# Optimization experiments

Hardware: AMD Instinct MI355X
Metric: run time of the kernel (lower is better)

Reference implementation:

```python
import jax, jax.numpy as jnp
import numpy as np
from jax.scipy.special import logsumexp

B, T, H, L = 64, 512, 768, 9


def setup_inputs() -> dict:
    key = jax.random.key(0)
    ks = jax.random.split(key, 8)
    length = jax.random.randint(ks[0], (B,), 0, T, dtype=jnp.int32)
    word2vec = jax.random.normal(ks[1], (B, T, H), dtype=jnp.float32)
    mask = jnp.ones((B, T), dtype=jnp.int32)
    label = jax.random.randint(ks[2], (B, T), 0, L, dtype=jnp.int32)
    # Linear(768 -> num_labels) params (PyTorch default init scale)
    bound = 1.0 / np.sqrt(H)
    W = jax.random.uniform(ks[3], (L, H), jnp.float32, -bound, bound)
    b = jax.random.uniform(ks[4], (L,), jnp.float32, -bound, bound)
    # CRF params (torchcrf init: uniform(-0.1, 0.1))
    start_transitions = jax.random.uniform(ks[5], (L,), jnp.float32, -0.1, 0.1)
    end_transitions = jax.random.uniform(ks[6], (L,), jnp.float32, -0.1, 0.1)
    transitions = jax.random.uniform(ks[7], (L, L), jnp.float32, -0.1, 0.1)
    return {"length": length, "word2vec": word2vec, "mask": mask, "label": label,
            "W": W, "b": b, "start_transitions": start_transitions,
            "end_transitions": end_transitions, "transitions": transitions}


def _crf_nll(emissions, tags, mask, start_transitions, end_transitions, transitions):
    # emissions [B,T,L], tags [B,T] int, mask [B,T] {0,1}
    Bn, Tn, Ln = emissions.shape
    maskf = mask.astype(emissions.dtype)
    # ---- numerator: score of the given tag sequence ----
    batch = jnp.arange(Bn)
    score = start_transitions[tags[:, 0]] + emissions[batch, 0, tags[:, 0]]
    # transition scores for steps 1..T-1, vectorized over time
    trans_sc = transitions[tags[:, :-1], tags[:, 1:]]                    # [B,T-1]
    emit_sc = jnp.take_along_axis(emissions, tags[..., None], axis=2)[..., 0]  # [B,T]
    score = score + jnp.sum((trans_sc + emit_sc[:, 1:]) * maskf[:, 1:], axis=1)
    seq_ends = jnp.sum(mask, axis=1).astype(jnp.int32) - 1
    last_tags = tags[batch, seq_ends]
    numerator = score + end_transitions[last_tags]
    # ---- denominator: log partition via forward algorithm (scan over time) ----
    em_t = jnp.transpose(emissions, (1, 0, 2))   # [T,B,L]
    mk_t = jnp.transpose(mask, (1, 0)) != 0      # [T,B]
    alpha0 = start_transitions[None, :] + em_t[0]  # [B,L]

    def step(alpha, inp):
        em_i, m_i = inp
        # alpha[b, i] + transitions[i, j] + emissions[b, j]
        nxt = logsumexp(alpha[:, :, None] + transitions[None, :, :] + em_i[:, None, :], axis=1)
        alpha = jnp.where(m_i[:, None], nxt, alpha)
        return alpha, None

    alpha, _ = jax.lax.scan(step, alpha0, (em_t[1:], mk_t[1:]))
    denominator = logsumexp(alpha + end_transitions[None, :], axis=1)
    llh = numerator - denominator
    return -jnp.mean(llh)


def reference(length, word2vec, mask, label, W, b, start_transitions, end_transitions, transitions):
    # dropout p=0.0 -> identity; Linear projection to emissions
    emissions = jnp.einsum('bth,lh->btl', word2vec, W) + b  # [B,T,L]
    return _crf_nll(emissions, label, mask, start_transitions, end_transitions, transitions)
```

## Files before the change

kernel.cpp:

```cpp
#include <hip/hip_runtime.h>
#include <hip/hip_bf16.h>


#define Bn 64
#define Tn 512
#define Hn 768
#define Ln 9
#define EMS 12
#define CS 16
#define NCHQ 8
#define QT 128
#define KSTEPS 24

typedef short bf16x8 __attribute__((ext_vector_type(8)));
typedef float f32x4  __attribute__((ext_vector_type(4)));

__device__ __forceinline__ short f2bf(float f) {
    return (short)__builtin_bit_cast(unsigned short, __float2bfloat16(f));
}

__global__ __launch_bounds__(512) void emis_q_kernel(
    const float* __restrict__ wv, const float* __restrict__ Wm,
    const float* __restrict__ bias, const int* __restrict__ mask,
    const int* __restrict__ label, const float* __restrict__ trans,
    const float* __restrict__ startT,
    float* __restrict__ Mq, float* __restrict__ lgq,
    float* __restrict__ numq, int* __restrict__ msq,
    float* __restrict__ em0, int* __restrict__ cnt)
{
    __shared__ bf16x8 wlds[KSTEPS * 64];
    __shared__ float  ldsE[QT][EMS];
    __shared__ int    ldsM[QT];
    __shared__ float  eTs[81];
    __shared__ float  sM[NCHQ][Ln][Ln];
    __shared__ float  sLg[NCHQ][Ln];
    __shared__ float  sp[8];
    __shared__ int    si[8];

    const int tid   = threadIdx.x;
    const int lane  = tid & 63;
    const int wid   = tid >> 6;
    const int bid   = blockIdx.x;
    const int b     = bid >> 2;
    const int q     = bid & 3;
    const int tbase = q * QT;

    if (bid == 0 && tid == 0) cnt[0] = 0;
    if (tid < 81) eTs[tid] = __expf(trans[tid]);

    for (int idx = tid; idx < KSTEPS * 64; idx += 512) {
        const int kk = idx >> 6, ln = idx & 63;
        const int n = ln & 15, kb2 = ln >> 4;
        bf16x8 v;
        if (n < Ln) {
            const float* src = Wm + n * Hn + kk * 32 + kb2 * 8;
#pragma unroll
            for (int j = 0; j < 8; ++j) v[j] = f2bf(src[j]);
        } else {
#pragma unroll
            for (int j = 0; j < 8; ++j) v[j] = 0;
        }
        wlds[idx] = v;
    }
    __syncthreads();

    {
        const int m  = lane & 15;
        const int kb = lane >> 4;
        const float* abase = wv + (size_t)(bid * QT + wid * 16 + m) * Hn + kb * 8;

        f32x4 acc = {0.f, 0.f, 0.f, 0.f};
#pragma unroll 4
        for (int kk = 0; kk < KSTEPS; ++kk) {
            float4 x0 = *reinterpret_cast<const float4*>(abase + kk * 32);
            float4 x1 = *reinterpret_cast<const float4*>(abase + kk * 32 + 4);
            bf16x8 a;
            a[0] = f2bf(x0.x); a[1] = f2bf(x0.y); a[2] = f2bf(x0.z); a[3] = f2bf(x0.w);
            a[4] = f2bf(x1.x); a[5] = f2bf(x1.y); a[6] = f2bf(x1.z); a[7] = f2bf(x1.w);
            bf16x8 bfr = wlds[kk * 64 + lane];
            acc = __builtin_amdgcn_mfma_f32_16x16x32_bf16(a, bfr, acc, 0, 0, 0);
        }
        const int l = lane & 15;
        if (l < Ln) {
            const float bl = bias[l];
#pragma unroll
            for (int r = 0; r < 4; ++r) {
                const int lrow = wid * 16 + (lane >> 4) * 4 + r;
                ldsE[lrow][l] = __expf(acc[r] + bl);
            }
        }
    }
    __syncthreads();

    float part = 0.f; int ms = 0;
    if (tid < QT) {
        const int gt  = tbase + tid;
        const int tag = label[b * Tn + gt];
        const int mk  = mask[b * Tn + gt];
        ldsM[tid] = mk; ms = mk;
        if (gt == 0) {
            part = startT[tag] + __logf(ldsE[0][tag]);
        } else if (mk) {
            const int prev = label[b * Tn + gt - 1];
            part = trans[prev * Ln + tag] + __logf(ldsE[tid][tag]);
        }
    }
#pragma unroll
    for (int off = 32; off > 0; off >>= 1) {
        part += __shfl_xor(part, off);
        ms   += __shfl_xor(ms, off);
    }
    if (lane == 0) { sp[wid] = part; si[wid] = ms; }
    __syncthreads();

    if (tid < NCHQ * Ln) {
        float Tr[81];
#pragma unroll
        for (int i = 0; i < 81; ++i) Tr[i] = eTs[i];
        const int r = tid % Ln;
        const int c = tid / Ln;

        float v[9];
#pragma unroll
        for (int k = 0; k < 9; ++k) v[k] = (k == r) ? 1.f : 0.f;
        float lg = 0.f;

        int t0 = tbase + c * CS; if (t0 == 0) t0 = 1;
        const int t1 = tbase + (c + 1) * CS;

        int lt = t0 - tbase;
        float4 e0v = *reinterpret_cast<const float4*>(&ldsE[lt][0]);
        float4 e1v = *reinterpret_cast<const float4*>(&ldsE[lt][4]);
        float  e8  = ldsE[lt][8];
        int    mk  = ldsM[lt];

        for (int t = t0; t < t1; ++t) {
            float4 p0 = make_float4(0.f, 0.f, 0.f, 0.f), p1 = p0;
            float  p8 = 0.f; int pm = 0;
            if (t + 1 < t1) {
                const int nlt = t + 1 - tbase;
                p0 = *reinterpret_cast<const float4*>(&ldsE[nlt][0]);
                p1 = *reinterpret_cast<const float4*>(&ldsE[nlt][4]);
                p8 = ldsE[nlt][8];
                pm = ldsM[nlt];
            }
            if (mk) {
                float e[9] = {e0v.x, e0v.y, e0v.z, e0v.w, e1v.x, e1v.y, e1v.z, e1v.w, e8};
                float nv[9];
#pragma unroll
                for (int jj = 0; jj < 9; ++jj) {
                    float acc = v[0] * Tr[jj];
#pragma unroll
                    for (int k = 1; k < 9; ++k) acc += v[k] * Tr[k * 9 + jj];
                    nv[jj] = acc * e[jj];
                }
                float mx = nv[0];
#pragma unroll
                for (int jj = 1; jj < 9; ++jj) mx = fmaxf(mx, nv[jj]);
                float inv = 1.f / mx;
#pragma unroll
                for (int jj = 0; jj < 9; ++jj) v[jj] = nv[jj] * inv;
                lg += __logf(mx);
            }
            e0v = p0; e1v = p1; e8 = p8; mk = pm;
        }
#pragma unroll
        for (int jj = 0; jj < 9; ++jj) sM[c][r][jj] = v[jj];
        sLg[c][r] = lg;
    }
    if (q == 0 && tid >= 72 && tid < 81) em0[b * Ln + (tid - 72)] = ldsE[0][tid - 72];
    if (tid == 100) {
        float s = 0.f; int m2 = 0;
#pragma unroll
        for (int i = 0; i < 8; ++i) { s += sp[i]; m2 += si[i]; }
        numq[bid] = s; msq[bid] = m2;
    }
    __syncthreads();

    for (int n = 4; n >= 2; n >>= 1) {
        float vout[9]; float lgout = 0.f;
        const bool act = tid < n * Ln;
        int p = 0, r = 0;
        if (act) {
            p = tid / Ln; r = tid % Ln;
            float mB = sLg[2 * p + 1][0];
#pragma unroll
            for (int k = 1; k < 9; ++k) mB = fmaxf(mB, sLg[2 * p + 1][k]);
            float tA[9];
#pragma unroll
            for (int k = 0; k < 9; ++k) tA[k] = sM[2 * p][r][k] * __expf(sLg[2 * p + 1][k] - mB);
#pragma unroll
            for (int jj = 0; jj < 9; ++jj) {
                float acc = tA[0] * sM[2 * p + 1][0][jj];
#pragma unroll
                for (int k = 1; k < 9; ++k) acc += tA[k] * sM[2 * p + 1][k][jj];
                vout[jj] = acc;
            }
            float mx = vout[0];
#pragma unroll
            for (int jj = 1; jj < 9; ++jj) mx = fmaxf(mx, vout[jj]);
            float inv = 1.f / mx;
#pragma unroll
            for (int jj = 0; jj < 9; ++jj) vout[jj] *= inv;
            lgout = sLg[2 * p][r] + mB + __logf(mx);
        }
        __syncthreads();
        if (act) {
#pragma unroll
            for (int jj = 0; jj < 9; ++jj) sM[p][r][jj] = vout[jj];
            sLg[p][r] = lgout;
        }
        __syncthreads();
    }

    if (tid < Ln) {
        const int r = tid;
        float mB = sLg[1][0];
#pragma unroll
        for (int k = 1; k < 9; ++k) mB = fmaxf(mB, sLg[1][k]);
        float tA[9];
#pragma unroll
        for (int k = 0; k < 9; ++k) tA[k] = sM[0][r][k] * __expf(sLg[1][k] - mB);
        float v[9];
#pragma unroll
        for (int jj = 0; jj < 9; ++jj) {
            float acc = tA[0] * sM[1][0][jj];
#pragma unroll
            for (int k = 1; k < 9; ++k) acc += tA[k] * sM[1][k][jj];
            v[jj] = acc;
        }
        float mx = v[0];
#pragma unroll
        for (int jj = 1; jj < 9; ++jj) mx = fmaxf(mx, v[jj]);
        float inv = 1.f / mx;
#pragma unroll
        for (int jj = 0; jj < 9; ++jj) Mq[bid * 81 + r * 9 + jj] = v[jj] * inv;
        lgq[bid * Ln + r] = sLg[0][r] + mB + __logf(mx);
    }
}

__global__ __launch_bounds__(64) void comb_kernel(
    const float* __restrict__ Mq, const float* __restrict__ lgq,
    const float* __restrict__ numq, const int* __restrict__ msq,
    const float* __restrict__ em0, const int* __restrict__ label,
    const float* __restrict__ startT, const float* __restrict__ endT,
    float* __restrict__ partial, int* __restrict__ cnt, float* __restrict__ out)
{
    __shared__ float cM[4][Ln][Ln];
    __shared__ float cLg[4][Ln];
    __shared__ float cem[Ln];
    __shared__ float cnum[4];
    __shared__ int   cms[4];

    const int b = blockIdx.x, tid = threadIdx.x;

    for (int i = tid; i < 4 * 81; i += 64) cM[i / 81][(i % 81) / 9][i % 9] = Mq[b * 324 + i];
    for (int i = tid; i < 4 * 9; i += 64)  cLg[i / 9][i % 9] = lgq[b * 36 + i];
    if (tid < Ln) cem[tid] = em0[b * Ln + tid];
    if (tid < 4) { cnum[tid] = numq[b * 4 + tid]; cms[tid] = msq[b * 4 + tid]; }
    __syncthreads();

    if (tid < 16) {
        const int lj = tid;
        const float NEG = -1e30f;
        float la = (lj < Ln) ? (startT[lj] + __logf(cem[lj])) : NEG;
        for (int c = 0; c < 4; ++c) {
            float mc[9];
#pragma unroll
            for (int rr = 0; rr < 9; ++rr) mc[rr] = (lj < Ln) ? cM[c][rr][lj] : 0.f;
            float x = (lj < Ln) ? (la + cLg[c][lj]) : NEG;
            float mm = x;
#pragma unroll
            for (int off = 1; off < 16; off <<= 1) mm = fmaxf(mm, __shfl_xor(mm, off, 16));
            float w = __expf(x - mm);
            float sacc = 0.f;
#pragma unroll
            for (int rr = 0; rr < 9; ++rr) sacc += __shfl(w, rr, 16) * mc[rr];
            la = (lj < Ln) ? (mm + __logf(sacc)) : NEG;
        }
        float x = (lj < Ln) ? (la + endT[lj]) : NEG;
        float mm = x;
#pragma unroll
        for (int off = 1; off < 16; off <<= 1) mm = fmaxf(mm, __shfl_xor(mm, off, 16));
        float se = __expf(x - mm);
#pragma unroll
        for (int off = 1; off < 16; off <<= 1) se += __shfl_xor(se, off, 16);
        if (lj == 0) {
            float denom = mm + __logf(se);
            float numer = cnum[0] + cnum[1] + cnum[2] + cnum[3];
            int   sm    = cms[0] + cms[1] + cms[2] + cms[3];
            int   last  = label[b * Tn + sm - 1];
            partial[b]  = denom - (numer + endT[last]);
        }
    }

    int old = 0;
    if (tid == 0) {
        __threadfence();
        old = atomicAdd(cnt, 1);
    }
    old = __shfl(old, 0);
    if (old == Bn - 1) {
        __threadfence();
        float pv = partial[tid];
#pragma unroll
        for (int off = 32; off > 0; off >>= 1) pv += __shfl_xor(pv, off);
        if (tid == 0) out[0] = pv * (1.0f / Bn);
    }
}

extern "C" void kernel_launch(void* const* d_in, const int* in_sizes, int n_in,
                              void* d_out, int out_size, void* d_ws, size_t ws_size,
                              hipStream_t stream)
{
    const float* wv    = (const float*)d_in[1];
    const int*   mask  = (const int*)d_in[2];
    const int*   label = (const int*)d_in[3];
    const float* Wm    = (const float*)d_in[4];
    const float* bias  = (const float*)d_in[5];
    const float* st    = (const float*)d_in[6];
    const float* en    = (const float*)d_in[7];
    const float* tr    = (const float*)d_in[8];

    float* ws      = (float*)d_ws;
    float* Mq      = ws;
    float* lgq     = ws + 20736;
    float* numq    = ws + 23040;
    int*   msq     = (int*)(ws + 23296);
    float* em0     = ws + 23552;
    float* partial = ws + 24128;
    int*   cnt     = (int*)(ws + 24192);
    float* out     = (float*)d_out;

    hipLaunchKernelGGL(emis_q_kernel, dim3(256), dim3(512), 0, stream,
                       wv, Wm, bias, mask, label, tr, st,
                       Mq, lgq, numq, msq, em0, cnt);
    hipLaunchKernelGGL(comb_kernel, dim3(Bn), dim3(64), 0, stream,
                       Mq, lgq, numq, msq, em0, label, st, en,
                       partial, cnt, out);
}
```

Before: 40.07 us.

## Split work into eighths and stream activations via async global-to-LDS triple buffer

Each batch row is now split into 8 blocks of 64 timesteps with 256 threads, doubling the block count so all CUs are covered. The activation loads now use global_load_lds into a swizzled, triple-buffered LDS ring with explicit waitcnt, which overlaps memory fetch with the MFMA projection. The chunk scan and tree combine are confined to wave 0 without block barriers, and the combine kernel gains one extra pairwise level. The cost is more LDS per block, more intermediate data in the workspace, and hand-written waitcnt counts that must match the issued loads exactly.

```diff
diff --git a/kernel.cpp b/kernel.cpp
--- a/kernel.cpp
+++ b/kernel.cpp
@@ -8,8 +8,8 @@
 #define Ln 9
 #define EMS 12
 #define CS 16
-#define NCHQ 8
-#define QT 128
+#define NCHO 4
+#define OT 64
 #define KSTEPS 24
 
 typedef short bf16x8 __attribute__((ext_vector_type(8)));
@@ -19,7 +19,40 @@
     return (short)__builtin_bit_cast(unsigned short, __float2bfloat16(f));
 }
 
-__global__ __launch_bounds__(512) void emis_q_kernel(
+#define GLOAD16(gp, lp)                                                        \
+    __builtin_amdgcn_global_load_lds(                                          \
+        (const __attribute__((address_space(1))) void*)(gp),                   \
+        (__attribute__((address_space(3))) void*)(lp), 16, 0, 0)
+
+__device__ __forceinline__ void pair_combine(
+    const float (*MA)[Ln], const float* lgA,
+    const float (*MB)[Ln], const float* lgB,
+    int r, float* outM, float* outLg)
+{
+    float mB = lgB[0];
+#pragma unroll
+    for (int k = 1; k < 9; ++k) mB = fmaxf(mB, lgB[k]);
+    float tA[9];
+#pragma unroll
+    for (int k = 0; k < 9; ++k) tA[k] = MA[r][k] * __expf(lgB[k] - mB);
+    float v[9];
+#pragma unroll
+    for (int jj = 0; jj < 9; ++jj) {
+        float acc = tA[0] * MB[0][jj];
+#pragma unroll
+        for (int k = 1; k < 9; ++k) acc += tA[k] * MB[k][jj];
+        v[jj] = acc;
+    }
+    float mx = v[0];
+#pragma unroll
+    for (int jj = 1; jj < 9; ++jj) mx = fmaxf(mx, v[jj]);
+    float inv = 1.f / mx;
+#pragma unroll
+    for (int jj = 0; jj < 9; ++jj) outM[jj] = v[jj] * inv;
+    *outLg = lgA[r] + mB + __logf(mx);
+}
+
+__global__ __launch_bounds__(256) void emis_o_kernel(
     const float* __restrict__ wv, const float* __restrict__ Wm,
     const float* __restrict__ bias, const int* __restrict__ mask,
     const int* __restrict__ label, const float* __restrict__ trans,
@@ -29,26 +62,27 @@
     float* __restrict__ em0, int* __restrict__ cnt)
 {
     __shared__ bf16x8 wlds[KSTEPS * 64];
-    __shared__ float  ldsE[QT][EMS];
-    __shared__ int    ldsM[QT];
-    __shared__ float  eTs[81];
-    __shared__ float  sM[NCHQ][Ln][Ln];
-    __shared__ float  sLg[NCHQ][Ln];
-    __shared__ float  sp[8];
-    __shared__ int    si[8];
+    __shared__ __align__(16) float bufA[4][3][512];
+    __shared__ float ldsE[OT][EMS];
+    __shared__ int   ldsM[OT];
+    __shared__ float eTs[81];
+    __shared__ float sM[NCHO][Ln][Ln];
+    __shared__ float sLg[NCHO][Ln];
+    __shared__ float s2M[2][Ln][Ln];
+    __shared__ float s2Lg[2][Ln];
 
     const int tid   = threadIdx.x;
     const int lane  = tid & 63;
     const int wid   = tid >> 6;
     const int bid   = blockIdx.x;
-    const int b     = bid >> 2;
-    const int q     = bid & 3;
-    const int tbase = q * QT;
+    const int b     = bid >> 3;
+    const int o     = bid & 7;
+    const int tbase = o * OT;
 
     if (bid == 0 && tid == 0) cnt[0] = 0;
     if (tid < 81) eTs[tid] = __expf(trans[tid]);
 
-    for (int idx = tid; idx < KSTEPS * 64; idx += 512) {
+    for (int idx = tid; idx < KSTEPS * 64; idx += 256) {
         const int kk = idx >> 6, ln = idx & 63;
         const int n = ln & 15, kb2 = ln >> 4;
         bf16x8 v;
@@ -65,21 +99,50 @@
     __syncthreads();
 
     {
+        const int rowbase = bid * OT + wid * 16;
+        const int rr   = lane >> 3;
+        const int colf = (((lane & 7) * 16) ^ (rr << 4)) >> 2;
+        const float* g0 = wv + (size_t)(rowbase + rr) * Hn + colf;
+        const float* g1 = g0 + 8 * Hn;
+        float* lb = &bufA[wid][0][0];
+
         const int m  = lane & 15;
         const int kb = lane >> 4;
-        const float* abase = wv + (size_t)(bid * QT + wid * 16 + m) * Hn + kb * 8;
+        const int ph0 = m * 32 + (((kb * 32)      ^ ((m & 7) << 4)) >> 2);
+        const int ph1 = m * 32 + (((kb * 32 + 16) ^ ((m & 7) << 4)) >> 2);
 
         f32x4 acc = {0.f, 0.f, 0.f, 0.f};
-#pragma unroll 4
-        for (int kk = 0; kk < KSTEPS; ++kk) {
-            float4 x0 = *reinterpret_cast<const float4*>(abase + kk * 32);
-            float4 x1 = *reinterpret_cast<const float4*>(abase + kk * 32 + 4);
-            bf16x8 a;
-            a[0] = f2bf(x0.x); a[1] = f2bf(x0.y); a[2] = f2bf(x0.z); a[3] = f2bf(x0.w);
-            a[4] = f2bf(x1.x); a[5] = f2bf(x1.y); a[6] = f2bf(x1.z); a[7] = f2bf(x1.w);
-            bf16x8 bfr = wlds[kk * 64 + lane];
-            acc = __builtin_amdgcn_mfma_f32_16x16x32_bf16(a, bfr, acc, 0, 0, 0);
-        }
+
+        GLOAD16(g0,      lb);        GLOAD16(g1,      lb + 256);
+        GLOAD16(g0 + 32, lb + 512);  GLOAD16(g1 + 32, lb + 768);
+
+#define EMIS_STEP(KK, SLOT)                                                    \
+        {                                                                      \
+            const float* s_ = lb + (SLOT) * 512;                               \
+            float4 x0 = *reinterpret_cast<const float4*>(s_ + ph0);            \
+            float4 x1 = *reinterpret_cast<const float4*>(s_ + ph1);            \
+            bf16x8 a;                                                          \
+            a[0] = f2bf(x0.x); a[1] = f2bf(x0.y);                              \
+            a[2] = f2bf(x0.z); a[3] = f2bf(x0.w);                              \
+            a[4] = f2bf(x1.x); a[5] = f2bf(x1.y);                              \
+            a[6] = f2bf(x1.z); a[7] = f2bf(x1.w);                              \
+            bf16x8 bfr = wlds[(KK) * 64 + lane];                               \
+            acc = __builtin_amdgcn_mfma_f32_16x16x32_bf16(a, bfr, acc, 0, 0, 0); \
+        }
+
+        for (int kk = 0; kk < KSTEPS - 2; ++kk) {
+            const int sl2 = (kk + 2) % 3;
+            GLOAD16(g0 + (kk + 2) * 32, lb + sl2 * 512);
+            GLOAD16(g1 + (kk + 2) * 32, lb + sl2 * 512 + 256);
+            asm volatile("s_waitcnt vmcnt(4)" ::: "memory");
+            EMIS_STEP(kk, kk % 3);
+        }
+        asm volatile("s_waitcnt vmcnt(2)" ::: "memory");
+        EMIS_STEP(KSTEPS - 2, (KSTEPS - 2) % 3);
+        asm volatile("s_waitcnt vmcnt(0)" ::: "memory");
+        EMIS_STEP(KSTEPS - 1, (KSTEPS - 1) % 3);
+#undef EMIS_STEP
+
         const int l = lane & 15;
         if (l < Ln) {
             const float bl = bias[l];
@@ -92,150 +155,101 @@
     }
     __syncthreads();
 
-    float part = 0.f; int ms = 0;
-    if (tid < QT) {
-        const int gt  = tbase + tid;
+    if (wid == 0) {
+        const int gt  = tbase + lane;
         const int tag = label[b * Tn + gt];
         const int mk  = mask[b * Tn + gt];
-        ldsM[tid] = mk; ms = mk;
+        ldsM[lane] = mk;
+        float part = 0.f; int ms = mk;
         if (gt == 0) {
             part = startT[tag] + __logf(ldsE[0][tag]);
         } else if (mk) {
             const int prev = label[b * Tn + gt - 1];
-            part = trans[prev * Ln + tag] + __logf(ldsE[tid][tag]);
-        }
-    }
-#pragma unroll
-    for (int off = 32; off > 0; off >>= 1) {
-        part += __shfl_xor(part, off);
-        ms   += __shfl_xor(ms, off);
-    }
-    if (lane == 0) { sp[wid] = part; si[wid] = ms; }
-    __syncthreads();
-
-    if (tid < NCHQ * Ln) {
-        float Tr[81];
-#pragma unroll
-        for (int i = 0; i < 81; ++i) Tr[i] = eTs[i];
-        const int r = tid % Ln;
-        const int c = tid / Ln;
-
-        float v[9];
-#pragma unroll
-        for (int k = 0; k < 9; ++k) v[k] = (k == r) ? 1.f : 0.f;
-        float lg = 0.f;
-
-        int t0 = tbase + c * CS; if (t0 == 0) t0 = 1;
-        const int t1 = tbase + (c + 1) * CS;
-
-        int lt = t0 - tbase;
-        float4 e0v = *reinterpret_cast<const float4*>(&ldsE[lt][0]);
-        float4 e1v = *reinterpret_cast<const float4*>(&ldsE[lt][4]);
-        float  e8  = ldsE[lt][8];
-        int    mk  = ldsM[lt];
-
-        for (int t = t0; t < t1; ++t) {
-            float4 p0 = make_float4(0.f, 0.f, 0.f, 0.f), p1 = p0;
-            float  p8 = 0.f; int pm = 0;
-            if (t + 1 < t1) {
-                const int nlt = t + 1 - tbase;
-                p0 = *reinterpret_cast<const float4*>(&ldsE[nlt][0]);
-                p1 = *reinterpret_cast<const float4*>(&ldsE[nlt][4]);
-                p8 = ldsE[nlt][8];
-                pm = ldsM[nlt];
+            part = trans[prev * Ln + tag] + __logf(ldsE[lane][tag]);
+        }
+#pragma unroll
+        for (int off = 32; off > 0; off >>= 1) {
+            part += __shfl_xor(part, off);
+            ms   += __shfl_xor(ms, off);
+        }
+        if (lane == 0) { numq[bid] = part; msq[bid] = ms; }
+        if (o == 0 && lane < Ln) em0[b * Ln + lane] = ldsE[0][lane];
+
+        if (tid < NCHO * Ln) {
+            float Tr[81];
+#pragma unroll
+            for (int i = 0; i < 81; ++i) Tr[i] = eTs[i];
+            const int r = tid % Ln;
+            const int c = tid / Ln;
+
+            float v[9];
+#pragma unroll
+            for (int k = 0; k < 9; ++k) v[k] = (k == r) ? 1.f : 0.f;
+            float lg = 0.f;
+
+            int t0 = tbase + c * CS; if (t0 == 0) t0 = 1;
+            const int t1 = tbase + (c + 1) * CS;
+
+            int lt = t0 - tbase;
+            float4 e0v = *reinterpret_cast<const float4*>(&ldsE[lt][0]);
+            float4 e1v = *reinterpret_cast<const float4*>(&ldsE[lt][4]);
+            float  e8  = ldsE[lt][8];
+            int    mk2 = ldsM[lt];
+
+            for (int t = t0; t < t1; ++t) {
+                float4 p0 = make_float4(0.f, 0.f, 0.f, 0.f), p1 = p0;
+                float  p8 = 0.f; int pm = 0;
+                if (t + 1 < t1) {
+                    const int nlt = t + 1 - tbase;
+                    p0 = *reinterpret_cast<const float4*>(&ldsE[nlt][0]);
+                    p1 = *reinterpret_cast<const float4*>(&ldsE[nlt][4]);
+                    p8 = ldsE[nlt][8];
+                    pm = ldsM[nlt];
+                }
+                if (mk2) {
+                    float e[9] = {e0v.x, e0v.y, e0v.z, e0v.w,
+                                  e1v.x, e1v.y, e1v.z, e1v.w, e8};
+                    float nv[9];
+#pragma unroll
+                    for (int jj = 0; jj < 9; ++jj) {
+                        float acc = v[0] * Tr[jj];
+#pragma unroll
+                        for (int k = 1; k < 9; ++k) acc += v[k] * Tr[k * 9 + jj];
+                        nv[jj] = acc * e[jj];
+                    }
+                    float mx = nv[0];
+#pragma unroll
+                    for (int jj = 1; jj < 9; ++jj) mx = fmaxf(mx, nv[jj]);
+                    float inv = 1.f / mx;
+#pragma unroll
+                    for (int jj = 0; jj < 9; ++jj) v[jj] = nv[jj] * inv;
+                    lg += __logf(mx);
+                }
+                e0v = p0; e1v = p1; e8 = p8; mk2 = pm;
             }
-            if (mk) {
-                float e[9] = {e0v.x, e0v.y, e0v.z, e0v.w, e1v.x, e1v.y, e1v.z, e1v.w, e8};
-                float nv[9];
-#pragma unroll
-                for (int jj = 0; jj < 9; ++jj) {
-                    float acc = v[0] * Tr[jj];
-#pragma unroll
-                    for (int k = 1; k < 9; ++k) acc += v[k] * Tr[k * 9 + jj];
-                    nv[jj] = acc * e[jj];
-                }
-                float mx = nv[0];
-#pragma unroll
-                for (int jj = 1; jj < 9; ++jj) mx = fmaxf(mx, nv[jj]);
-                float inv = 1.f / mx;
-#pragma unroll
-                for (int jj = 0; jj < 9; ++jj) v[jj] = nv[jj] * inv;
-                lg += __logf(mx);
-            }
-            e0v = p0; e1v = p1; e8 = p8; mk = pm;
-        }
-#pragma unroll
-        for (int jj = 0; jj < 9; ++jj) sM[c][r][jj] = v[jj];
-        sLg[c][r] = lg;
-    }
-    if (q == 0 && tid >= 72 && tid < 81) em0[b * Ln + (tid - 72)] = ldsE[0][tid - 72];
-    if (tid == 100) {
-        float s = 0.f; int m2 = 0;
-#pragma unroll
-        for (int i = 0; i < 8; ++i) { s += sp[i]; m2 += si[i]; }
-        numq[bid] = s; msq[bid] = m2;
-    }
-    __syncthreads();
-
-    for (int n = 4; n >= 2; n >>= 1) {
-        float vout[9]; float lgout = 0.f;
-        const bool act = tid < n * Ln;
-        int p = 0, r = 0;
-        if (act) {
-            p = tid / Ln; r = tid % Ln;
-            float mB = sLg[2 * p + 1][0];
-#pragma unroll
-            for (int k = 1; k < 9; ++k) mB = fmaxf(mB, sLg[2 * p + 1][k]);
-            float tA[9];
-#pragma unroll
-            for (int k = 0; k < 9; ++k) tA[k] = sM[2 * p][r][k] * __expf(sLg[2 * p + 1][k] - mB);
-#pragma unroll
-            for (int jj = 0; jj < 9; ++jj) {
-                float acc = tA[0] * sM[2 * p + 1][0][jj];
-#pragma unroll
-                for (int k = 1; k < 9; ++k) acc += tA[k] * sM[2 * p + 1][k][jj];
-                vout[jj] = acc;
-            }
-            float mx = vout[0];
-#pragma unroll
-            for (int jj = 1; jj < 9; ++jj) mx = fmaxf(mx, vout[jj]);
-            float inv = 1.f / mx;
-#pragma unroll
-            for (int jj = 0; jj < 9; ++jj) vout[jj] *= inv;
-            lgout = sLg[2 * p][r] + mB + __logf(mx);
-        }
-        __syncthreads();
-        if (act) {
-#pragma unroll
-            for (int jj = 0; jj < 9; ++jj) sM[p][r][jj] = vout[jj];
-            sLg[p][r] = lgout;
-        }
-        __syncthreads();
-    }
-
-    if (tid < Ln) {
-        const int r = tid;
-        float mB = sLg[1][0];
-#pragma unroll
-        for (int k = 1; k < 9; ++k) mB = fmaxf(mB, sLg[1][k]);
-        float tA[9];
-#pragma unroll
-        for (int k = 0; k < 9; ++k) tA[k] = sM[0][r][k] * __expf(sLg[1][k] - mB);
-        float v[9];
-#pragma unroll
-        for (int jj = 0; jj < 9; ++jj) {
-            float acc = tA[0] * sM[1][0][jj];
-#pragma unroll
-            for (int k = 1; k < 9; ++k) acc += tA[k] * sM[1][k][jj];
-            v[jj] = acc;
-        }
-        float mx = v[0];
-#pragma unroll
-        for (int jj = 1; jj < 9; ++jj) mx = fmaxf(mx, v[jj]);
-        float inv = 1.f / mx;
-#pragma unroll
-        for (int jj = 0; jj < 9; ++jj) Mq[bid * 81 + r * 9 + jj] = v[jj] * inv;
-        lgq[bid * Ln + r] = sLg[0][r] + mB + __logf(mx);
+#pragma unroll
+            for (int jj = 0; jj < 9; ++jj) sM[c][r][jj] = v[jj];
+            sLg[c][r] = lg;
+        }
+
+        if (tid < 2 * Ln) {
+            const int p = tid / Ln, r = tid % Ln;
+            float om[9], ol;
+            pair_combine(sM[2 * p], sLg[2 * p], sM[2 * p + 1], sLg[2 * p + 1],
+                         r, om, &ol);
+#pragma unroll
+            for (int jj = 0; jj < 9; ++jj) s2M[p][r][jj] = om[jj];
+            s2Lg[p][r] = ol;
+        }
+
+        if (tid < Ln) {
+            const int r = tid;
+            float om[9], ol;
+            pair_combine(s2M[0], s2Lg[0], s2M[1], s2Lg[1], r, om, &ol);
+#pragma unroll
+            for (int jj = 0; jj < 9; ++jj) Mq[bid * 81 + r * 9 + jj] = om[jj];
+            lgq[bid * Ln + r] = ol;
+        }
     }
 }
 
@@ -246,18 +260,31 @@
     const float* __restrict__ startT, const float* __restrict__ endT,
     float* __restrict__ partial, int* __restrict__ cnt, float* __restrict__ out)
 {
-    __shared__ float cM[4][Ln][Ln];
-    __shared__ float cLg[4][Ln];
+    __shared__ float cO[8][Ln][Ln];
+    __shared__ float cOl[8][Ln];
+    __shared__ float cQ[4][Ln][Ln];
+    __shared__ float cQl[4][Ln];
     __shared__ float cem[Ln];
-    __shared__ float cnum[4];
-    __shared__ int   cms[4];
+    __shared__ float cnum[8];
+    __shared__ int   cms[8];
 
     const int b = blockIdx.x, tid = threadIdx.x;
 
-    for (int i = tid; i < 4 * 81; i += 64) cM[i / 81][(i % 81) / 9][i % 9] = Mq[b * 324 + i];
-    for (int i = tid; i < 4 * 9; i += 64)  cLg[i / 9][i % 9] = lgq[b * 36 + i];
+    for (int i = tid; i < 8 * 81; i += 64) ((float*)cO)[i]  = Mq[b * 648 + i];
+    for (int i = tid; i < 8 * 9;  i += 64) ((float*)cOl)[i] = lgq[b * 72 + i];
     if (tid < Ln) cem[tid] = em0[b * Ln + tid];
-    if (tid < 4) { cnum[tid] = numq[b * 4 + tid]; cms[tid] = msq[b * 4 + tid]; }
+    if (tid < 8) { cnum[tid] = numq[b * 8 + tid]; cms[tid] = msq[b * 8 + tid]; }
+    __syncthreads();
+
+    if (tid < 4 * Ln) {
+        const int p = tid / Ln, r = tid % Ln;
+        float om[9], ol;
+        pair_combine(cO[2 * p], cOl[2 * p], cO[2 * p + 1], cOl[2 * p + 1],
+                     r, om, &ol);
+#pragma unroll
+        for (int jj = 0; jj < 9; ++jj) cQ[p][r][jj] = om[jj];
+        cQl[p][r] = ol;
+    }
     __syncthreads();
 
     if (tid < 16) {
@@ -267,8 +294,8 @@
         for (int c = 0; c < 4; ++c) {
             float mc[9];
 #pragma unroll
-            for (int rr = 0; rr < 9; ++rr) mc[rr] = (lj < Ln) ? cM[c][rr][lj] : 0.f;
-            float x = (lj < Ln) ? (la + cLg[c][lj]) : NEG;
+            for (int rr = 0; rr < 9; ++rr) mc[rr] = (lj < Ln) ? cQ[c][rr][lj] : 0.f;
+            float x = (lj < Ln) ? (la + cQl[c][lj]) : NEG;
             float mm = x;
 #pragma unroll
             for (int off = 1; off < 16; off <<= 1) mm = fmaxf(mm, __shfl_xor(mm, off, 16));
@@ -287,8 +314,10 @@
         for (int off = 1; off < 16; off <<= 1) se += __shfl_xor(se, off, 16);
         if (lj == 0) {
             float denom = mm + __logf(se);
-            float numer = cnum[0] + cnum[1] + cnum[2] + cnum[3];
-            int   sm    = cms[0] + cms[1] + cms[2] + cms[3];
+            float numer = cnum[0] + cnum[1] + cnum[2] + cnum[3]
+                        + cnum[4] + cnum[5] + cnum[6] + cnum[7];
+            int   sm    = cms[0] + cms[1] + cms[2] + cms[3]
+                        + cms[4] + cms[5] + cms[6] + cms[7];
             int   last  = label[b * Tn + sm - 1];
             partial[b]  = denom - (numer + endT[last]);
         }
@@ -324,15 +353,15 @@
 
     float* ws      = (float*)d_ws;
     float* Mq      = ws;
-    float* lgq     = ws + 20736;
-    float* numq    = ws + 23040;
-    int*   msq     = (int*)(ws + 23296);
-    float* em0     = ws + 23552;
-    float* partial = ws + 24128;
-    int*   cnt     = (int*)(ws + 24192);
+    float* lgq     = ws + 41472;
+    float* numq    = ws + 46080;
+    int*   msq     = (int*)(ws + 46592);
+    float* em0     = ws + 47104;
+    float* partial = ws + 47680;
+    int*   cnt     = (int*)(ws + 47744);
     float* out     = (float*)d_out;
 
-    hipLaunchKernelGGL(emis_q_kernel, dim3(256), dim3(512), 0, stream,
+    hipLaunchKernelGGL(emis_o_kernel, dim3(512), dim3(256), 0, stream,
                        wv, Wm, bias, mask, label, tr, st,
                        Mq, lgq, numq, msq, em0, cnt);
     hipLaunchKernelGGL(comb_kernel, dim3(Bn), dim3(64), 0, stream,
```

Result: slower. 42.21 us (+5.3%).

## Fuse combine kernel into main kernel via last-block atomic counter

Applied to the files above, without the earlier changes.

Removes the separate combine kernel launch. Each block increments a global counter with release semantics, and the last block to arrive does the per-sequence chunk combination for all 64 batches and the final mean reduction. A hipMemsetAsync resets the counter before launch. The intent is to drop a kernel launch and the gap between kernels. The cost is that a single block serializes the combine work, and the memset adds its own operation to the stream.

```diff
diff --git a/kernel.cpp b/kernel.cpp
--- a/kernel.cpp
+++ b/kernel.cpp
@@ -11,6 +11,7 @@
 #define NCHQ 8
 #define QT 128
 #define KSTEPS 24
+#define NBLKS 256
 
 typedef short bf16x8 __attribute__((ext_vector_type(8)));
 typedef float f32x4  __attribute__((ext_vector_type(4)));
@@ -23,10 +24,11 @@
     const float* __restrict__ wv, const float* __restrict__ Wm,
     const float* __restrict__ bias, const int* __restrict__ mask,
     const int* __restrict__ label, const float* __restrict__ trans,
-    const float* __restrict__ startT,
+    const float* __restrict__ startT, const float* __restrict__ endT,
     float* __restrict__ Mq, float* __restrict__ lgq,
     float* __restrict__ numq, int* __restrict__ msq,
-    float* __restrict__ em0, int* __restrict__ cnt)
+    float* __restrict__ em0, int* __restrict__ cnt,
+    float* __restrict__ out)
 {
     __shared__ bf16x8 wlds[KSTEPS * 64];
     __shared__ float  ldsE[QT][EMS];
@@ -36,6 +38,8 @@
     __shared__ float  sLg[NCHQ][Ln];
     __shared__ float  sp[8];
     __shared__ int    si[8];
+    __shared__ float  nllArr[Bn];
+    __shared__ int    sOld;
 
     const int tid   = threadIdx.x;
     const int lane  = tid & 63;
@@ -45,7 +49,6 @@
     const int q     = bid & 3;
     const int tbase = q * QT;
 
-    if (bid == 0 && tid == 0) cnt[0] = 0;
     if (tid < 81) eTs[tid] = __expf(trans[tid]);
 
     for (int idx = tid; idx < KSTEPS * 64; idx += 512) {
@@ -237,72 +240,65 @@
         for (int jj = 0; jj < 9; ++jj) Mq[bid * 81 + r * 9 + jj] = v[jj] * inv;
         lgq[bid * Ln + r] = sLg[0][r] + mB + __logf(mx);
     }
-}
-
-__global__ __launch_bounds__(64) void comb_kernel(
-    const float* __restrict__ Mq, const float* __restrict__ lgq,
-    const float* __restrict__ numq, const int* __restrict__ msq,
-    const float* __restrict__ em0, const int* __restrict__ label,
-    const float* __restrict__ startT, const float* __restrict__ endT,
-    float* __restrict__ partial, int* __restrict__ cnt, float* __restrict__ out)
-{
-    __shared__ float cM[4][Ln][Ln];
-    __shared__ float cLg[4][Ln];
-    __shared__ float cem[Ln];
-    __shared__ float cnum[4];
-    __shared__ int   cms[4];
-
-    const int b = blockIdx.x, tid = threadIdx.x;
-
-    for (int i = tid; i < 4 * 81; i += 64) cM[i / 81][(i % 81) / 9][i % 9] = Mq[b * 324 + i];
-    for (int i = tid; i < 4 * 9; i += 64)  cLg[i / 9][i % 9] = lgq[b * 36 + i];
-    if (tid < Ln) cem[tid] = em0[b * Ln + tid];
-    if (tid < 4) { cnum[tid] = numq[b * 4 + tid]; cms[tid] = msq[b * 4 + tid]; }
-    __syncthreads();
-
-    if (tid < 16) {
-        const int lj = tid;
+
+    __syncthreads();
+    if (tid == 0) {
+        sOld = __hip_atomic_fetch_add(cnt, 1, __ATOMIC_RELEASE,
+                                      __HIP_MEMORY_SCOPE_AGENT);
+    }
+    __syncthreads();
+    if (sOld != NBLKS - 1) return;
+
+    if (tid == 0) {
+        (void)__hip_atomic_load(cnt, __ATOMIC_ACQUIRE, __HIP_MEMORY_SCOPE_AGENT);
+    }
+    __syncthreads();
+
+    {
+        const int lj = tid & 15;
+        const int g  = tid >> 4;
         const float NEG = -1e30f;
-        float la = (lj < Ln) ? (startT[lj] + __logf(cem[lj])) : NEG;
-        for (int c = 0; c < 4; ++c) {
-            float mc[9];
-#pragma unroll
-            for (int rr = 0; rr < 9; ++rr) mc[rr] = (lj < Ln) ? cM[c][rr][lj] : 0.f;
-            float x = (lj < Ln) ? (la + cLg[c][lj]) : NEG;
+#pragma unroll
+        for (int pass = 0; pass < 2; ++pass) {
+            const int bb = g + pass * 32;
+            float la = (lj < Ln) ? (startT[lj] + __logf(em0[bb * Ln + lj])) : NEG;
+            for (int c = 0; c < 4; ++c) {
+                const float* Mc = Mq + (bb * 4 + c) * 81;
+                float mc[9];
+#pragma unroll
+                for (int rr = 0; rr < 9; ++rr) mc[rr] = (lj < Ln) ? Mc[rr * 9 + lj] : 0.f;
+                float x = (lj < Ln) ? (la + lgq[(bb * 4 + c) * Ln + lj]) : NEG;
+                float mm = x;
+#pragma unroll
+                for (int off = 1; off < 16; off <<= 1) mm = fmaxf(mm, __shfl_xor(mm, off, 16));
+                float w = __expf(x - mm);
+                float sacc = 0.f;
+#pragma unroll
+                for (int rr = 0; rr < 9; ++rr) sacc += __shfl(w, rr, 16) * mc[rr];
+                la = (lj < Ln) ? (mm + __logf(sacc)) : NEG;
+            }
+            float x = (lj < Ln) ? (la + endT[lj]) : NEG;
             float mm = x;
 #pragma unroll
             for (int off = 1; off < 16; off <<= 1) mm = fmaxf(mm, __shfl_xor(mm, off, 16));
-            float w = __expf(x - mm);
-            float sacc = 0.f;
-#pragma unroll
-            for (int rr = 0; rr < 9; ++rr) sacc += __shfl(w, rr, 16) * mc[rr];
-            la = (lj < Ln) ? (mm + __logf(sacc)) : NEG;
-        }
-        float x = (lj < Ln) ? (la + endT[lj]) : NEG;
-        float mm = x;
-#pragma unroll
-        for (int off = 1; off < 16; off <<= 1) mm = fmaxf(mm, __shfl_xor(mm, off, 16));
-        float se = __expf(x - mm);
-#pragma unroll
-        for (int off = 1; off < 16; off <<= 1) se += __shfl_xor(se, off, 16);
-        if (lj == 0) {
-            float denom = mm + __logf(se);
-            float numer = cnum[0] + cnum[1] + cnum[2] + cnum[3];
-            int   sm    = cms[0] + cms[1] + cms[2] + cms[3];
-            int   last  = label[b * Tn + sm - 1];
-            partial[b]  = denom - (numer + endT[last]);
-        }
-    }
-
-    int old = 0;
-    if (tid == 0) {
-        __threadfence();
-        old = atomicAdd(cnt, 1);
-    }
-    old = __shfl(old, 0);
-    if (old == Bn - 1) {
-        __threadfence();
-        float pv = partial[tid];
+            float se = __expf(x - mm);
+#pragma unroll
+            for (int off = 1; off < 16; off <<= 1) se += __shfl_xor(se, off, 16);
+            if (lj == 0) {
+                float denom = mm + __logf(se);
+                float numer = numq[bb * 4 + 0] + numq[bb * 4 + 1]
+                            + numq[bb * 4 + 2] + numq[bb * 4 + 3];
+                int   sm    = msq[bb * 4 + 0] + msq[bb * 4 + 1]
+                            + msq[bb * 4 + 2] + msq[bb * 4 + 3];
+                int   last  = label[bb * Tn + sm - 1];
+                nllArr[bb]  = denom - (numer + endT[last]);
+            }
+        }
+    }
+    __syncthreads();
+
+    if (tid < 64) {
+        float pv = nllArr[tid];
 #pragma unroll
         for (int off = 32; off > 0; off >>= 1) pv += __shfl_xor(pv, off);
         if (tid == 0) out[0] = pv * (1.0f / Bn);
@@ -328,14 +324,12 @@
     float* numq    = ws + 23040;
     int*   msq     = (int*)(ws + 23296);
     float* em0     = ws + 23552;
-    float* partial = ws + 24128;
-    int*   cnt     = (int*)(ws + 24192);
+    int*   cnt     = (int*)(ws + 24128);
     float* out     = (float*)d_out;
 
-    hipLaunchKernelGGL(emis_q_kernel, dim3(256), dim3(512), 0, stream,
-                       wv, Wm, bias, mask, label, tr, st,
-                       Mq, lgq, numq, msq, em0, cnt);
-    hipLaunchKernelGGL(comb_kernel, dim3(Bn), dim3(64), 0, stream,
-                       Mq, lgq, numq, msq, em0, label, st, en,
-                       partial, cnt, out);
+    hipMemsetAsync(cnt, 0, sizeof(int), stream);
+
+    hipLaunchKernelGGL(emis_q_kernel, dim3(NBLKS), dim3(512), 0, stream,
+                       wv, Wm, bias, mask, label, tr, st, en,
+                       Mq, lgq, numq, msq, em0, cnt, out);
 }
```

Result: slower. 49.74 us (+24.1%).
